# Kernel tuning notes

Measured on AMD Instinct MI355X. Metric: run time of the kernel, lower is better.

The kernel has to match this reference:

```python
import jax, jax.numpy as jnp
import numpy as np

B, L, H = 256, 2048, 64

def _min_gru(x, Wz, bz, Wh, bh):
    # x: [B, L, Din] -> h: [B, L, H] via parallel scan of h_t = (1-z_t)*h_{t-1} + z_t*h~_t, h_0 = 0
    z = jax.nn.sigmoid(jnp.einsum('bli,ih->blh', x, Wz) + bz)
    h_tilde = jnp.einsum('bli,ih->blh', x, Wh) + bh
    a = 1.0 - z
    b = z * h_tilde
    def combine(c1, c2):
        a1, b1 = c1
        a2, b2 = c2
        return a1 * a2, b1 * a2 + b2
    _, h = jax.lax.associative_scan(combine, (a, b), axis=1)
    return h

def _stacked(x, Wz0, bz0, Wh0, bh0, Wz1, bz1, Wh1, bh1, Wo, bo):
    h = _min_gru(x, Wz0, bz0, Wh0, bh0)
    h = _min_gru(h, Wz1, bz1, Wh1, bh1)
    return jnp.einsum('blh,ho->blo', h, Wo) + bo  # [B, L, 1]

def setup_inputs():
    key = jax.random.key(0)
    ks = jax.random.split(key, 32)
    inputs = jax.random.bernoulli(ks[0], 0.5, (B, L)).astype(jnp.float32)
    p_array = jax.random.permutation(ks[1], L).astype(jnp.int32)
    def lin(k, fin, fout):
        return (jax.random.normal(k, (fin, fout), jnp.float32) / np.float32(np.sqrt(fin)))
    d = {'inputs': inputs, 'p_array': p_array}
    i = 2
    for r in (1, 2):
        for nm, fin, fout in (('z0', 1, H), ('h0', 1, H), ('z1', H, H), ('h1', H, H), ('o', H, 1)):
            d['w%d%s' % (r, nm)] = lin(ks[i], fin, fout); i += 1
            d['b%d%s' % (r, nm)] = jnp.zeros((fout,), jnp.float32)
    return d

def reference(inputs, p_array, w1z0, b1z0, w1h0, b1h0, w1z1, b1z1, w1h1, b1h1, w1o, b1o,
              w2z0, b2z0, w2h0, b2h0, w2z1, b2z1, w2h1, b2h1, w2o, b2o):
    x = inputs[..., None]                      # [B, L, 1]
    x_sys = _stacked(x, w1z0, b1z0, w1h0, b1h0, w1z1, b1z1, w1h1, b1h1, w1o, b1o)
    x_int = x[:, p_array, :]                   # interleave along sequence dim
    x_p1 = _stacked(x_int, w2z0, b2z0, w2h0, b2h0, w2z1, b2z1, w2h1, b2h1, w2o, b2o)
    x_tx = jnp.concatenate([x_sys, x_p1], axis=2)  # [B, L, 2]
    mean = jnp.mean(x_tx)
    std = jnp.std(x_tx, ddof=1)                # torch.std is unbiased by default
    return (x_tx - mean) / std                 # squeeze(dim=2) is a no-op on size-2 dim
```

## Files before the change

### kernel.cpp

```cpp
#include <hip/hip_runtime.h>

#define BB 256
#define LL 2048
#define HH 64
#define TT 64
#define SS 68
#define NCH (LL / TT)
#define NTOT (BB * LL * 2)

typedef __attribute__((ext_vector_type(8))) short bf16x8;
typedef __attribute__((ext_vector_type(4))) float f32x4;

__device__ __forceinline__ float rcp_(float x) { return __builtin_amdgcn_rcpf(x); }

__device__ __forceinline__ short f2bf_rne(float f) {
    union { float f; unsigned u; } v; v.f = f;
    unsigned r = v.u + 0x7fff + ((v.u >> 16) & 1);
    return (short)(r >> 16);
}

template<int CTRL>
__device__ __forceinline__ float qdpp(float x) {
    union { float f; int i; } u, r;
    u.f = x;
    r.i = __builtin_amdgcn_update_dpp(0, u.i, CTRL, 0xF, 0xF, false);
    return r.f;
}

__device__ __forceinline__ void load_x(const float* __restrict__ xrow,
                                       const int* __restrict__ p,
                                       bool pm, int tb, float* xv)
{
    if (!pm) {
        const float4* x4 = (const float4*)(xrow + tb);
        #pragma unroll
        for (int k = 0; k < 4; ++k) {
            const float4 v = x4[k];
            xv[4*k+0] = v.x; xv[4*k+1] = v.y; xv[4*k+2] = v.z; xv[4*k+3] = v.w;
        }
    } else {
        const int4* p4 = (const int4*)(p + tb);
        int idx[16];
        #pragma unroll
        for (int k = 0; k < 4; ++k) {
            const int4 v = p4[k];
            idx[4*k+0] = v.x; idx[4*k+1] = v.y; idx[4*k+2] = v.z; idx[4*k+3] = v.w;
        }
        #pragma unroll
        for (int i = 0; i < 16; ++i) xv[i] = xrow[idx[i]];
    }
}

__device__ __forceinline__ void p1_scan(const float* xv,
                                        float a0v, float b0v, float a1v, float b1v,
                                        int seg, int col0, float& carry, float* sh)
{
    float ai[16], bi[16];
    float A = 1.0f, Bv = 0.0f;
    #pragma unroll
    for (int i = 0; i < 16; ++i) {
        const bool on = (xv[i] != 0.0f);
        ai[i] = on ? a1v : a0v;
        bi[i] = on ? b1v : b0v;
        A  = A * ai[i];
        Bv = fmaf(Bv, ai[i], bi[i]);
    }
    {
        const float Au = qdpp<0x90>(A), Bu = qdpp<0x90>(Bv);
        if (seg >= 1) { const float Ac = A; A = Au * Ac; Bv = fmaf(Bu, Ac, Bv); }
        const float Au2 = qdpp<0x44>(A), Bu2 = qdpp<0x44>(Bv);
        if (seg >= 2) { const float Ac = A; A = Au2 * Ac; Bv = fmaf(Bu2, Ac, Bv); }
    }
    float Ae = qdpp<0x90>(A), Be = qdpp<0x90>(Bv);
    if (seg == 0) { Ae = 1.0f; Be = 0.0f; }
    float cc = fmaf(Ae, carry, Be);
    #pragma unroll
    for (int i = 0; i < 16; ++i) {
        cc = fmaf(ai[i], cc, bi[i]);
        sh[(seg * 16 + i) * SS + col0] = cc;
    }
    carry = qdpp<0xFF>(cc);
}

__global__ void __launch_bounds__(256)
__attribute__((amdgpu_waves_per_eu(2, 2)))
gru_fused(const float* __restrict__ x, const int* __restrict__ p,
               const float* __restrict__ w1z0, const float* __restrict__ b1z0,
               const float* __restrict__ w1h0, const float* __restrict__ b1h0,
               const float* __restrict__ w1z1, const float* __restrict__ b1z1,
               const float* __restrict__ w1h1, const float* __restrict__ b1h1,
               const float* __restrict__ w1o,  const float* __restrict__ b1o,
               const float* __restrict__ w2z0, const float* __restrict__ b2z0,
               const float* __restrict__ w2h0, const float* __restrict__ b2h0,
               const float* __restrict__ w2z1, const float* __restrict__ b2z1,
               const float* __restrict__ w2h1, const float* __restrict__ b2h1,
               const float* __restrict__ w2o,  const float* __restrict__ b2o,
               float* __restrict__ out, float* __restrict__ ws)
{
    const int  b  = blockIdx.x;
    const bool pm = (blockIdx.y != 0);

    const float* wz0 = pm ? w2z0 : w1z0;
    const float* bz0 = pm ? b2z0 : b1z0;
    const float* wh0 = pm ? w2h0 : w1h0;
    const float* bh0 = pm ? b2h0 : b1h0;
    const float* wz1 = pm ? w2z1 : w1z1;
    const float* bz1 = pm ? b2z1 : b1z1;
    const float* wh1 = pm ? w2h1 : w1h1;
    const float* bh1 = pm ? b2h1 : b1h1;
    const float* wo  = pm ? w2o  : w1o;
    const float* bov = pm ? b2o  : b1o;

    const int tid  = threadIdx.x;
    const int lane = tid & 63;
    const int tg   = tid >> 6;
    const int q    = lane >> 4;
    const int n    = lane & 15;
    const int seg  = lane & 3;
    const int hidx = (tg << 4) | (lane >> 2);

    __shared__ __align__(16) float s_h[2 * TT * SS];
    __shared__ float2 s_w[2][4][HH];
    __shared__ float s_red[8];

    const float* xrow = x + (size_t)b * LL;

    const float z0v = rcp_(1.0f + __expf(-bz0[hidx]));
    const float z1v = rcp_(1.0f + __expf(-(wz0[hidx] + bz0[hidx])));
    const float a0v = 1.0f - z0v, b0v = z0v * bh0[hidx];
    const float a1v = 1.0f - z1v, b1v = z1v * (wh0[hidx] + bh0[hidx]);

    float rbz1[4], rbh1[4], rwo4[4];
    #pragma unroll
    for (int ht = 0; ht < 4; ++ht) {
        rbz1[ht] = bz1[ht * 16 + n];
        rbh1[ht] = bh1[ht * 16 + n];
        rwo4[ht] = wo[ht * 16 + n];
    }
    const float bo = bov[0];

    bf16x8 wfz[2][4], wfh[2][4];
    for (int ks = 0; ks < 2; ++ks) {
        for (int ht = 0; ht < 4; ++ht) {
            #pragma unroll
            for (int j = 0; j < 8; ++j) {
                const int kk = ks * 32 + q * 8 + j;
                const int hh = ht * 16 + n;
                wfz[ks][ht][j] = f2bf_rne(wz1[kk * HH + hh]);
                wfh[ks][ht][j] = f2bf_rne(wh1[kk * HH + hh]);
            }
        }
    }

    float carry0 = 0.0f;
    float carry1[4] = {0.0f, 0.0f, 0.0f, 0.0f};
    f32x4 ga[4], gb[4];
    float Aqe[4], Bqe[4];
    float lsum = 0.0f, lsum2 = 0.0f;
    float* outp = out + (pm ? 1 : 0);
    const int t0 = tg * 16;
    const int col0 = hidx ^ ((seg & 1) << 4);

    float xv[16];

    auto g2_step = [&](int cm) {
        const int buf = cm & 1;
        float Acm[4] = {1,1,1,1}, Bcm[4] = {0,0,0,0};
        float Ap[4], Bp[4];
        #pragma unroll
        for (int w = 0; w < 4; ++w) {
            #pragma unroll
            for (int ht = 0; ht < 4; ++ht) {
                if (w == tg) { Ap[ht] = Acm[ht]; Bp[ht] = Bcm[ht]; }
                const float2 ab = s_w[buf][w][ht * 16 + n];
                Bcm[ht] = fmaf(ab.x, Bcm[ht], ab.y);
                Acm[ht] *= ab.x;
            }
        }
        float vo[4] = {0,0,0,0};
        #pragma unroll
        for (int ht = 0; ht < 4; ++ht) {
            float cc = fmaf(Aqe[ht], fmaf(Ap[ht], carry1[ht], Bp[ht]), Bqe[ht]);
            #pragma unroll
            for (int r = 0; r < 4; ++r) {
                cc = fmaf(ga[ht][r], cc, gb[ht][r]);
                vo[r] = fmaf(cc, rwo4[ht], vo[r]);
            }
            carry1[ht] = fmaf(Acm[ht], carry1[ht], Bcm[ht]);
        }
        #pragma unroll
        for (int m = 1; m <= 8; m <<= 1) {
            #pragma unroll
            for (int r = 0; r < 4; ++r) vo[r] += __shfl_xor(vo[r], m);
        }
        if (n == 0) {
            #pragma unroll
            for (int r = 0; r < 4; ++r) {
                const float v = vo[r] + bo;
                outp[((size_t)b * LL + cm * TT + t0 + q * 4 + r) * 2] = v;
                lsum += v;
                lsum2 = fmaf(v, v, lsum2);
            }
        }
    };

    load_x(xrow, p, pm, seg * 16, xv);
    p1_scan(xv, a0v, b0v, a1v, b1v, seg, col0, carry0, s_h);
    __syncthreads();

    for (int c = 0; c < NCH; ++c) {
        const int cp1 = c + 1;

        if (cp1 < NCH)
            load_x(xrow, p, pm, cp1 * TT + seg * 16, xv);

        if (c > 0) g2_step(c - 1);

        {
            #pragma unroll
            for (int ht = 0; ht < 4; ++ht) {
                ga[ht] = (f32x4){rbz1[ht], rbz1[ht], rbz1[ht], rbz1[ht]};
                gb[ht] = (f32x4){rbh1[ht], rbh1[ht], rbh1[ht], rbh1[ht]};
            }
            const float* shR = s_h + (c & 1) * (TT * SS);
            const int qs = q ^ ((tg & 1) << 1);
            #pragma unroll
            for (int ks = 0; ks < 2; ++ks) {
                const float* ap = &shR[(t0 + n) * SS + ks * 32 + qs * 8];
                const float4 av0 = *(const float4*)ap;
                const float4 av1 = *(const float4*)(ap + 4);
                float af[8] = {av0.x, av0.y, av0.z, av0.w, av1.x, av1.y, av1.z, av1.w};
                bf16x8 ahi, alo;
                #pragma unroll
                for (int j = 0; j < 8; ++j) {
                    union { float f; unsigned u; } uf; uf.f = af[j];
                    ahi[j] = (short)(uf.u >> 16);
                    union { unsigned u; float f; } hf; hf.u = uf.u & 0xffff0000u;
                    const float rem = af[j] - hf.f;
                    union { float f; unsigned u; } ur; ur.f = rem;
                    alo[j] = (short)(ur.u >> 16);
                }
                #pragma unroll
                for (int ht = 0; ht < 4; ++ht) {
                    ga[ht] = __builtin_amdgcn_mfma_f32_16x16x32_bf16(ahi, wfz[ks][ht], ga[ht], 0, 0, 0);
                    ga[ht] = __builtin_amdgcn_mfma_f32_16x16x32_bf16(alo, wfz[ks][ht], ga[ht], 0, 0, 0);
                    gb[ht] = __builtin_amdgcn_mfma_f32_16x16x32_bf16(ahi, wfh[ks][ht], gb[ht], 0, 0, 0);
                    gb[ht] = __builtin_amdgcn_mfma_f32_16x16x32_bf16(alo, wfh[ks][ht], gb[ht], 0, 0, 0);
                }
            }
            #pragma unroll
            for (int ht = 0; ht < 4; ++ht) {
                #pragma unroll
                for (int r = 0; r < 4; ++r) {
                    const float v  = ga[ht][r];
                    const float e  = __expf(-v);
                    const float r1 = rcp_(1.0f + e);
                    ga[ht][r] = e * r1;
                    gb[ht][r] = r1 * gb[ht][r];
                }
            }
            float Aq[4], Bq[4];
            #pragma unroll
            for (int ht = 0; ht < 4; ++ht) {
                float A = 1.0f, B = 0.0f;
                #pragma unroll
                for (int r = 0; r < 4; ++r) {
                    B = fmaf(ga[ht][r], B, gb[ht][r]);
                    A = A * ga[ht][r];
                }
                Aq[ht] = A; Bq[ht] = B;
            }
            #pragma unroll
            for (int ht = 0; ht < 4; ++ht) {
                const float Au = __shfl_up(Aq[ht], 16), Bu = __shfl_up(Bq[ht], 16);
                if (q >= 1) { const float Ac = Aq[ht]; Aq[ht] = Ac * Au; Bq[ht] = fmaf(Ac, Bu, Bq[ht]); }
            }
            #pragma unroll
            for (int ht = 0; ht < 4; ++ht) {
                const float Au = __shfl_up(Aq[ht], 32), Bu = __shfl_up(Bq[ht], 32);
                if (q >= 2) { const float Ac = Aq[ht]; Aq[ht] = Ac * Au; Bq[ht] = fmaf(Ac, Bu, Bq[ht]); }
            }
            #pragma unroll
            for (int ht = 0; ht < 4; ++ht) {
                const float Ae = __shfl_up(Aq[ht], 16), Be = __shfl_up(Bq[ht], 16);
                Aqe[ht] = (q == 0) ? 1.0f : Ae;
                Bqe[ht] = (q == 0) ? 0.0f : Be;
            }
            if (q == 3) {
                #pragma unroll
                for (int ht = 0; ht < 4; ++ht)
                    s_w[c & 1][tg][ht * 16 + n] = make_float2(Aq[ht], Bq[ht]);
            }
        }

        if (cp1 < NCH)
            p1_scan(xv, a0v, b0v, a1v, b1v, seg, col0, carry0,
                    s_h + (cp1 & 1) * (TT * SS));

        __syncthreads();
    }

    g2_step(NCH - 1);

    #pragma unroll
    for (int o = 32; o; o >>= 1) {
        lsum  += __shfl_down(lsum, o);
        lsum2 += __shfl_down(lsum2, o);
    }
    if (lane == 0) { s_red[tg] = lsum; s_red[4 + tg] = lsum2; }
    __syncthreads();
    if (tid == 0) {
        const int gb2 = b * 2 + (pm ? 1 : 0);
        ws[2 * gb2]     = s_red[0] + s_red[1] + s_red[2] + s_red[3];
        ws[2 * gb2 + 1] = s_red[4] + s_red[5] + s_red[6] + s_red[7];
    }
}

__global__ void normalize_k(float* __restrict__ out, const float* __restrict__ ws)
{
    __shared__ float s_red[8];
    float s = 0.0f, s2 = 0.0f;
    for (int i = threadIdx.x; i < 2 * BB; i += 256) {
        s  += ws[2 * i];
        s2 += ws[2 * i + 1];
    }
    #pragma unroll
    for (int o = 32; o; o >>= 1) {
        s  += __shfl_down(s, o);
        s2 += __shfl_down(s2, o);
    }
    const int wid = threadIdx.x >> 6;
    if ((threadIdx.x & 63) == 0) { s_red[wid] = s; s_red[4 + wid] = s2; }
    __syncthreads();
    const float tot  = s_red[0] + s_red[1] + s_red[2] + s_red[3];
    const float tot2 = s_red[4] + s_red[5] + s_red[6] + s_red[7];
    const float N    = (float)NTOT;
    const float mean = tot / N;
    const float var  = (tot2 - N * mean * mean) / (N - 1.0f);
    const float inv  = rsqrtf(var);

    const int i = blockIdx.x * blockDim.x + threadIdx.x;
    float4* o4 = (float4*)out;
    float4 v = o4[i];
    v.x = (v.x - mean) * inv;
    v.y = (v.y - mean) * inv;
    v.z = (v.z - mean) * inv;
    v.w = (v.w - mean) * inv;
    o4[i] = v;
}

extern "C" void kernel_launch(void* const* d_in, const int* in_sizes, int n_in,
                              void* d_out, int out_size, void* d_ws, size_t ws_size,
                              hipStream_t stream)
{
    (void)in_sizes; (void)n_in; (void)out_size; (void)ws_size;
    const float* x = (const float*)d_in[0];
    const int*   p = (const int*)d_in[1];
    float* out = (float*)d_out;
    float* ws  = (float*)d_ws;

    dim3 grid(BB, 2);
    gru_fused<<<grid, 256, 0, stream>>>(
        x, p,
        (const float*)d_in[2],  (const float*)d_in[3],
        (const float*)d_in[4],  (const float*)d_in[5],
        (const float*)d_in[6],  (const float*)d_in[7],
        (const float*)d_in[8],  (const float*)d_in[9],
        (const float*)d_in[10], (const float*)d_in[11],
        (const float*)d_in[12], (const float*)d_in[13],
        (const float*)d_in[14], (const float*)d_in[15],
        (const float*)d_in[16], (const float*)d_in[17],
        (const float*)d_in[18], (const float*)d_in[19],
        (const float*)d_in[20], (const float*)d_in[21],
        out, ws);

    normalize_k<<<NTOT / 4 / 256, 256, 0, stream>>>(out, ws);
}
```

Before: 212.6 us.

## Stage input row in LDS upfront, use DPP row reductions, simplify sigmoid gate math

New measurement: 185.5 us. 1.15x faster.

```diff
diff --git a/kernel.cpp b/kernel.cpp
--- a/kernel.cpp
+++ b/kernel.cpp
@@ -27,39 +27,29 @@
     return r.f;
 }
 
-__device__ __forceinline__ void load_x(const float* __restrict__ xrow,
-                                       const int* __restrict__ p,
-                                       bool pm, int tb, float* xv)
-{
-    if (!pm) {
-        const float4* x4 = (const float4*)(xrow + tb);
-        #pragma unroll
-        for (int k = 0; k < 4; ++k) {
-            const float4 v = x4[k];
-            xv[4*k+0] = v.x; xv[4*k+1] = v.y; xv[4*k+2] = v.z; xv[4*k+3] = v.w;
-        }
-    } else {
-        const int4* p4 = (const int4*)(p + tb);
-        int idx[16];
-        #pragma unroll
-        for (int k = 0; k < 4; ++k) {
-            const int4 v = p4[k];
-            idx[4*k+0] = v.x; idx[4*k+1] = v.y; idx[4*k+2] = v.z; idx[4*k+3] = v.w;
-        }
-        #pragma unroll
-        for (int i = 0; i < 16; ++i) xv[i] = xrow[idx[i]];
-    }
-}
-
-__device__ __forceinline__ void p1_scan(const float* xv,
+template<int D>
+__device__ __forceinline__ float rshr(float x) {
+    union { float f; int i; } u, r;
+    u.f = x;
+    r.i = __builtin_amdgcn_update_dpp(0, u.i, 0x110 | D, 0xF, 0xF, true);
+    return r.f;
+}
+
+__device__ __forceinline__ void p1_scan(const float* __restrict__ sxp,
                                         float a0v, float b0v, float a1v, float b1v,
                                         int seg, int col0, float& carry, float* sh)
 {
+    float xi[16];
+    #pragma unroll
+    for (int k = 0; k < 4; ++k) {
+        const float4 v = *(const float4*)(sxp + 4 * k);
+        xi[4*k+0] = v.x; xi[4*k+1] = v.y; xi[4*k+2] = v.z; xi[4*k+3] = v.w;
+    }
     float ai[16], bi[16];
     float A = 1.0f, Bv = 0.0f;
     #pragma unroll
     for (int i = 0; i < 16; ++i) {
-        const bool on = (xv[i] != 0.0f);
+        const bool on = (xi[i] != 0.0f);
         ai[i] = on ? a1v : a0v;
         bi[i] = on ? b1v : b0v;
         A  = A * ai[i];
@@ -120,10 +110,29 @@
     const int hidx = (tg << 4) | (lane >> 2);
 
     __shared__ __align__(16) float s_h[2 * TT * SS];
+    __shared__ __align__(16) float s_x[LL];
     __shared__ float2 s_w[2][4][HH];
     __shared__ float s_red[8];
 
     const float* xrow = x + (size_t)b * LL;
+
+    if (!pm) {
+        const float4* x4 = (const float4*)xrow;
+        float4* sx4 = (float4*)s_x;
+        #pragma unroll
+        for (int i = 0; i < LL / 4 / 256; ++i)
+            sx4[tid + 256 * i] = x4[tid + 256 * i];
+    } else {
+        const int4* p4 = (const int4*)p;
+        float4* sx4 = (float4*)s_x;
+        #pragma unroll
+        for (int i = 0; i < LL / 4 / 256; ++i) {
+            const int4 v = p4[tid + 256 * i];
+            float4 w;
+            w.x = xrow[v.x]; w.y = xrow[v.y]; w.z = xrow[v.z]; w.w = xrow[v.w];
+            sx4[tid + 256 * i] = w;
+        }
+    }
 
     const float z0v = rcp_(1.0f + __expf(-bz0[hidx]));
     const float z1v = rcp_(1.0f + __expf(-(wz0[hidx] + bz0[hidx])));
@@ -161,8 +170,6 @@
     const int t0 = tg * 16;
     const int col0 = hidx ^ ((seg & 1) << 4);
 
-    float xv[16];
-
     auto g2_step = [&](int cm) {
         const int buf = cm & 1;
         float Acm[4] = {1,1,1,1}, Bcm[4] = {0,0,0,0};
@@ -189,11 +196,13 @@
             carry1[ht] = fmaf(Acm[ht], carry1[ht], Bcm[ht]);
         }
         #pragma unroll
-        for (int m = 1; m <= 8; m <<= 1) {
-            #pragma unroll
-            for (int r = 0; r < 4; ++r) vo[r] += __shfl_xor(vo[r], m);
-        }
-        if (n == 0) {
+        for (int r = 0; r < 4; ++r) {
+            vo[r] += rshr<1>(vo[r]);
+            vo[r] += rshr<2>(vo[r]);
+            vo[r] += rshr<4>(vo[r]);
+            vo[r] += rshr<8>(vo[r]);
+        }
+        if (n == 15) {
             #pragma unroll
             for (int r = 0; r < 4; ++r) {
                 const float v = vo[r] + bo;
@@ -204,15 +213,13 @@
         }
     };
 
-    load_x(xrow, p, pm, seg * 16, xv);
-    p1_scan(xv, a0v, b0v, a1v, b1v, seg, col0, carry0, s_h);
+    __syncthreads();
+
+    p1_scan(s_x + seg * 16, a0v, b0v, a1v, b1v, seg, col0, carry0, s_h);
     __syncthreads();
 
     for (int c = 0; c < NCH; ++c) {
         const int cp1 = c + 1;
-
-        if (cp1 < NCH)
-            load_x(xrow, p, pm, cp1 * TT + seg * 16, xv);
 
         if (c > 0) g2_step(c - 1);
 
@@ -252,11 +259,11 @@
             for (int ht = 0; ht < 4; ++ht) {
                 #pragma unroll
                 for (int r = 0; r < 4; ++r) {
-                    const float v  = ga[ht][r];
-                    const float e  = __expf(-v);
-                    const float r1 = rcp_(1.0f + e);
-                    ga[ht][r] = e * r1;
-                    gb[ht][r] = r1 * gb[ht][r];
+                    const float v   = ga[ht][r];
+                    const float a   = rcp_(1.0f + __expf(v));
+                    const float htl = gb[ht][r];
+                    ga[ht][r] = a;
+                    gb[ht][r] = fmaf(-a, htl, htl);
                 }
             }
             float Aq[4], Bq[4];
@@ -294,7 +301,7 @@
         }
 
         if (cp1 < NCH)
-            p1_scan(xv, a0v, b0v, a1v, b1v, seg, col0, carry0,
+            p1_scan(s_x + cp1 * TT + seg * 16, a0v, b0v, a1v, b1v, seg, col0, carry0,
                     s_h + (cp1 & 1) * (TT * SS));
 
         __syncthreads();
```
